# Performance work log

Hardware: AMD Instinct MI355X
Metric: run time of the kernel (lower is better)

Reference implementation:

```python
import jax, jax.numpy as jnp
from jax import lax
import numpy as np

H = 64  # hidden_dim


def _lstm_dir(x, W_ih, W_hh, b, reverse):
    # x: [B,T,I]; W_ih: [4H,I]; W_hh: [4H,H]; b: [4H] (b_ih+b_hh combined)
    B = x.shape[0]
    xp = jnp.einsum('bti,gi->btg', x, W_ih) + b          # [B,T,4H]
    xp = jnp.swapaxes(xp, 0, 1)                          # [T,B,4H]

    def step(carry, xt):
        h, c = carry
        g = xt + h @ W_hh.T                              # [B,4H]
        i, f, gg, o = jnp.split(g, 4, axis=-1)           # PyTorch gate order i,f,g,o
        i = jax.nn.sigmoid(i)
        f = jax.nn.sigmoid(f)
        gg = jnp.tanh(gg)
        o = jax.nn.sigmoid(o)
        c = f * c + i * gg
        h = o * jnp.tanh(c)
        return (h, c), h

    init = (jnp.zeros((B, H), x.dtype), jnp.zeros((B, H), x.dtype))
    _, hs = lax.scan(step, init, xp, reverse=reverse)    # outputs aligned to original positions
    return jnp.swapaxes(hs, 0, 1)                        # [B,T,H]


def _bilstm_layer(x, Wih_f, Whh_f, b_f, Wih_b, Whh_b, b_b):
    fwd = _lstm_dir(x, Wih_f, Whh_f, b_f, reverse=False)
    bwd = _lstm_dir(x, Wih_b, Whh_b, b_b, reverse=True)
    return jnp.concatenate([fwd, bwd], axis=-1)          # [B,T,2H]


def setup_inputs() -> dict:
    key = jax.random.key(0)
    ks = jax.random.split(key, 16)
    s = 0.1
    d = {}
    d['x'] = jax.random.normal(ks[0], (512, 512, 4), dtype=jnp.float32)
    # layer 0 (input size 4), forward / backward directions
    d['Wih_l0_f'] = jax.random.normal(ks[1], (4 * H, 4)) * s
    d['Whh_l0_f'] = jax.random.normal(ks[2], (4 * H, H)) * s
    d['b_l0_f'] = jax.random.normal(ks[3], (4 * H,)) * s
    d['Wih_l0_b'] = jax.random.normal(ks[4], (4 * H, 4)) * s
    d['Whh_l0_b'] = jax.random.normal(ks[5], (4 * H, H)) * s
    d['b_l0_b'] = jax.random.normal(ks[6], (4 * H,)) * s
    # layer 1 (input size 2H = 128)
    d['Wih_l1_f'] = jax.random.normal(ks[7], (4 * H, 2 * H)) * s
    d['Whh_l1_f'] = jax.random.normal(ks[8], (4 * H, H)) * s
    d['b_l1_f'] = jax.random.normal(ks[9], (4 * H,)) * s
    d['Wih_l1_b'] = jax.random.normal(ks[10], (4 * H, 2 * H)) * s
    d['Whh_l1_b'] = jax.random.normal(ks[11], (4 * H, H)) * s
    d['b_l1_b'] = jax.random.normal(ks[12], (4 * H,)) * s
    # final linear: 2H -> 1
    d['fc_w'] = jax.random.normal(ks[13], (1, 2 * H)) * s
    d['fc_b'] = jax.random.normal(ks[14], (1,)) * s
    return d


def reference(x, Wih_l0_f, Whh_l0_f, b_l0_f, Wih_l0_b, Whh_l0_b, b_l0_b,
              Wih_l1_f, Whh_l1_f, b_l1_f, Wih_l1_b, Whh_l1_b, b_l1_b,
              fc_w, fc_b):
    h0 = _bilstm_layer(x, Wih_l0_f, Whh_l0_f, b_l0_f, Wih_l0_b, Whh_l0_b, b_l0_b)
    h1 = _bilstm_layer(h0, Wih_l1_f, Whh_l1_f, b_l1_f, Wih_l1_b, Whh_l1_b, b_l1_b)
    pooled = jnp.mean(h1, axis=1)                        # [B,2H]
    return pooled @ fc_w.T + fc_b                        # [B,1]
```

## Files before the change

### kernel.cpp

```cpp
#include <hip/hip_runtime.h>

#define H  64
#define TT 512
#define BB 512
#define CSTR 80
#define UCH 16
#define XROW 264
#define XCH  (UCH * XROW + 8)
#define NCHUNK (TT / UCH)

typedef _Float16 half8 __attribute__((ext_vector_type(8)));
typedef float    f32x4 __attribute__((ext_vector_type(4)));

#define LOG2E 1.4426950408889634f
#define TWOL  2.8853900817779268f
#define FOURL 5.7707801635558536f

#define MFMA16 __builtin_amdgcn_mfma_f32_16x16x32_f16

__device__ __forceinline__ float frcp(float x) { return __builtin_amdgcn_rcpf(x); }
__device__ __forceinline__ float ex2(float x)  { return __builtin_amdgcn_exp2f(x); }

__device__ __forceinline__ void step_barrier() {
    asm volatile("s_waitcnt lgkmcnt(0)\n\ts_barrier" ::: "memory");
}

__device__ __forceinline__ float sel4(f32x4 v, bool lo, bool hi) {
    float a = lo ? v[1] : v[0];
    float b = lo ? v[3] : v[2];
    return hi ? b : a;
}

__global__ __launch_bounds__(256) void xpad_prep(const float* __restrict__ x,
                                                 _Float16* __restrict__ xpad) {
    int gid = blockIdx.x * 256 + threadIdx.x;
    int row = gid >> 2, q = gid & 3;
    half8 v = {0,0,0,0,0,0,0,0};
    if (q == 0) {
        float4 xv = ((const float4*)x)[row];
        v[0] = (_Float16)xv.x; v[1] = (_Float16)xv.y;
        v[2] = (_Float16)xv.z; v[3] = (_Float16)xv.w;
    }
    *(half8*)(xpad + (size_t)row * 32 + q * 8) = v;
}


#define L0_CHUNK(CIDX, XPR, XPW, AUSE, ALOAD)                                   \
    {                                                                           \
        const int c_ = (CIDX);                                                  \
        if (c_ + 2 < NCHUNK) {                                                  \
            const int tL = dir ? (TT - 1 - ((c_ + 2) * UCH + m))                \
                               : ((c_ + 2) * UCH + m);                          \
            _Pragma("unroll")                                                   \
            for (int cc = 0; cc < 4; ++cc)                                      \
                ALOAD[cc] = *(const half8*)(xpad +                              \
                    (size_t)((b0 + cc) * TT + tL) * 32 + q * 8);                \
        }                                                                       \
        _Pragma("unroll")                                                       \
        for (int u = 0; u < UCH; ++u) {                                         \
            half8 ah0 = *(const half8*)&hbuf[p][ch][q * 8];                     \
            half8 ah1 = *(const half8*)&hbuf[p][ch][32 + q * 8];                \
            f32x4 xq = *(const f32x4*)&XPR[ch * XCH + u * XROW + uo * 4];       \
            f32x4 g0 = MFMA16(Ah[0][0], ah0, vz, 0, 0, 0);                      \
            g0       = MFMA16(Ah[0][1], ah1, g0, 0, 0, 0);                      \
            f32x4 g1 = MFMA16(Ah[1][0], ah0, vz, 0, 0, 0);                      \
            g1       = MFMA16(Ah[1][1], ah1, g1, 0, 0, 0);                      \
            f32x4 g2 = MFMA16(Ah[2][0], ah0, vz, 0, 0, 0);                      \
            g2       = MFMA16(Ah[2][1], ah1, g2, 0, 0, 0);                      \
            f32x4 g3 = MFMA16(Ah[3][0], ah0, vz, 0, 0, 0);                      \
            g3       = MFMA16(Ah[3][1], ah1, g3, 0, 0, 0);                      \
            {                                \
                f32x4 acc = bb[u & 3];                                          \
                acc = MFMA16(Wg[u & 3], AUSE[u >> 2], acc, 0, 0, 0);            \
                *(f32x4*)&XPW[(u >> 2) * XCH + m * XROW +                       \
                              (w * 16 + (u & 3) * 4 + q) * 4] = acc;            \
            }                                                                   \
            float gi = sel4(g0, sLo, sHi) + xq[0];                              \
            float gf = sel4(g1, sLo, sHi) + xq[1];                              \
            float gg = sel4(g2, sLo, sHi) + xq[2];                              \
            float go = sel4(g3, sLo, sHi) + xq[3];                              \
            float e_i = frcp(1.f + ex2(gi));                                    \
            float e_f = frcp(1.f + ex2(gf));                                    \
            float tg  = TWOL - FOURL * frcp(1.f + ex2(gg));                     \
            float e_o = frcp(1.f + ex2(go));                                    \
            cp = e_f * cp + e_i * tg;                                           \
            float hh = e_o * fmaf(-2.f, frcp(1.f + ex2(cp)), 1.f);              \
            const int tg_t = dir ? (TT - 1 - (c_ * UCH + u)) : (c_ * UCH + u);  \
            out0[((size_t)(b0 + ch) * TT + tg_t) * 128 + dir * 64 + uo] =       \
                (_Float16)hh;                                                   \
            hbuf[p ^ 1][ch][uo] = (_Float16)hh;                                 \
            step_barrier();                                                     \
            p ^= 1;                                                             \
        }                                                                       \
    }

__global__ __launch_bounds__(256, 1) void lstm_l0(
    const _Float16* __restrict__ xpad,
    const float* __restrict__ WihF, const float* __restrict__ WhhF, const float* __restrict__ bF,
    const float* __restrict__ WihB, const float* __restrict__ WhhB, const float* __restrict__ bB,
    _Float16* __restrict__ out0)
{
    const int dir = blockIdx.x & 1;
    const int b0  = (blockIdx.x >> 1) * 4;
    const int tid = threadIdx.x;
    const int w = tid >> 6, l = tid & 63, m = l & 15, q = l >> 4;
    const int ch = m & 3;
    const int i0 = m >> 2;
    const int uo = w * 16 + q * 4 + i0;
    const bool sLo = (i0 & 1) != 0, sHi = (i0 & 2) != 0;

    const float* Wih = dir ? WihB : WihF;
    const float* Whh = dir ? WhhB : WhhF;
    const float* bia = dir ? bB   : bF;

    half8 Ah[4][2];
#pragma unroll
    for (int t = 0; t < 4; ++t) {
        const float st = (t == 2) ? TWOL : -LOG2E;
        const int wrow = t * 64 + w * 16 + m;
#pragma unroll
        for (int s2 = 0; s2 < 2; ++s2) {
            const float* src = Whh + wrow * 64 + s2 * 32 + q * 8;
            half8 tmp;
#pragma unroll
            for (int j = 0; j < 8; ++j) tmp[j] = (_Float16)(src[j] * st);
            Ah[t][s2] = tmp;
        }
    }

    const float sm = ((m & 3) == 2) ? TWOL : -LOG2E;
    half8 Wg[4];
#pragma unroll
    for (int j = 0; j < 4; ++j) {
        const int gr = (m & 3) * 64 + w * 16 + j * 4 + (m >> 2);
        half8 tmp;
#pragma unroll
        for (int jj = 0; jj < 8; ++jj) {
            int k = q * 8 + jj;
            tmp[jj] = (k < 4) ? (_Float16)(Wih[gr * 4 + k] * sm) : (_Float16)0.f;
        }
        Wg[j] = tmp;
    }

    f32x4 bb[4];
#pragma unroll
    for (int j = 0; j < 4; ++j) {
        const int ub = w * 16 + j * 4 + q;
        bb[j][0] = bia[ub]       * -LOG2E;
        bb[j][1] = bia[64 + ub]  * -LOG2E;
        bb[j][2] = bia[128 + ub] * TWOL;
        bb[j][3] = bia[192 + ub] * -LOG2E;
    }

    const f32x4 vz = {0.f, 0.f, 0.f, 0.f};

    __shared__ __align__(16) float xpA[4 * XCH];
    __shared__ __align__(16) float xpB[4 * XCH];
    __shared__ __align__(16) _Float16 hbuf[2][4][CSTR];
    for (int i = tid; i < 2 * 4 * CSTR / 2; i += 256) ((unsigned int*)hbuf)[i] = 0u;

    float cp = 0.f;
    int p = 0;

    half8 aR[2][4];
    {
        const int t0 = dir ? (TT - 1 - m) : m;
        const int t1 = dir ? (TT - 1 - (UCH + m)) : (UCH + m);
#pragma unroll
        for (int cc = 0; cc < 4; ++cc) {
            aR[0][cc] = *(const half8*)(xpad + (size_t)((b0 + cc) * TT + t0) * 32 + q * 8);
            aR[1][cc] = *(const half8*)(xpad + (size_t)((b0 + cc) * TT + t1) * 32 + q * 8);
        }
#pragma unroll
        for (int pp = 0; pp < 16; ++pp) {
            const int cc = pp >> 2, j = pp & 3;
            f32x4 acc = bb[j];
            acc = MFMA16(Wg[j], aR[0][cc], acc, 0, 0, 0);
            *(f32x4*)&xpA[cc * XCH + m * XROW + (w * 16 + j * 4 + q) * 4] = acc;
        }
        __syncthreads();
    }

    for (int c = 0; c < NCHUNK; c += 2) {
        L0_CHUNK(c,     xpA, xpB, aR[1], aR[0]);
        L0_CHUNK(c + 1, xpB, xpA, aR[0], aR[1]);
    }
}

#define L1_CHUNK(CIDX, XPR, XPW, AUSE, ALOAD)                                   \
    {                                                                           \
        const int c_ = (CIDX);                                                  \
        if (c_ + 2 < NCHUNK) {                                                  \
            const int tL = dir ? (TT - 1 - ((c_ + 2) * UCH + m))                \
                               : ((c_ + 2) * UCH + m);                          \
            _Pragma("unroll")                                                   \
            for (int cc = 0; cc < 4; ++cc) {                                    \
                const _Float16* arow = out0 +                                   \
                    (size_t)((b0 + cc) * TT + tL) * 128 + q * 8;                \
                _Pragma("unroll")                                               \
                for (int k4 = 0; k4 < 4; ++k4)                                  \
                    ALOAD[cc][k4] = *(const half8*)(arow + k4 * 32);            \
            }                                                                   \
        }                                                                       \
        _Pragma("unroll")                                                       \
        for (int u = 0; u < UCH; ++u) {                                         \
            half8 ah0 = *(const half8*)&hbuf[p][ch][q * 8];                     \
            half8 ah1 = *(const half8*)&hbuf[p][ch][32 + q * 8];                \
            f32x4 xq = *(const f32x4*)&XPR[ch * XCH + u * XROW + uo * 4];       \
            f32x4 g0 = MFMA16(Ah[0][0], ah0, vz, 0, 0, 0);                      \
            g0       = MFMA16(Ah[0][1], ah1, g0, 0, 0, 0);                      \
            f32x4 g1 = MFMA16(Ah[1][0], ah0, vz, 0, 0, 0);                      \
            g1       = MFMA16(Ah[1][1], ah1, g1, 0, 0, 0);                      \
            f32x4 g2 = MFMA16(Ah[2][0], ah0, vz, 0, 0, 0);                      \
            g2       = MFMA16(Ah[2][1], ah1, g2, 0, 0, 0);                      \
            f32x4 g3 = MFMA16(Ah[3][0], ah0, vz, 0, 0, 0);                      \
            g3       = MFMA16(Ah[3][1], ah1, g3, 0, 0, 0);                      \
            {                                   \
                f32x4 acc = bb[u & 3];                                          \
                acc = MFMA16(Wg[u & 3][0], AUSE[u >> 2][0], acc, 0, 0, 0);      \
                acc = MFMA16(Wg[u & 3][1], AUSE[u >> 2][1], acc, 0, 0, 0);      \
                acc = MFMA16(Wg[u & 3][2], AUSE[u >> 2][2], acc, 0, 0, 0);      \
                acc = MFMA16(Wg[u & 3][3], AUSE[u >> 2][3], acc, 0, 0, 0);      \
                *(f32x4*)&XPW[(u >> 2) * XCH + m * XROW +                       \
                              (w * 16 + (u & 3) * 4 + q) * 4] = acc;            \
            }                                                                   \
            float gi = sel4(g0, sLo, sHi) + xq[0];                              \
            float gf = sel4(g1, sLo, sHi) + xq[1];                              \
            float gg = sel4(g2, sLo, sHi) + xq[2];                              \
            float go = sel4(g3, sLo, sHi) + xq[3];                              \
            float e_i = frcp(1.f + ex2(gi));                                    \
            float e_f = frcp(1.f + ex2(gf));                                    \
            float tg  = TWOL - FOURL * frcp(1.f + ex2(gg));                     \
            float e_o = frcp(1.f + ex2(go));                                    \
            cp = e_f * cp + e_i * tg;                                           \
            float hh = e_o * fmaf(-2.f, frcp(1.f + ex2(cp)), 1.f);              \
            hs += hh;                                                           \
            hbuf[p ^ 1][ch][uo] = (_Float16)hh;                                 \
            step_barrier();                                                     \
            p ^= 1;                                                             \
        }                                                                       \
    }

__global__ __launch_bounds__(256, 1) void lstm_l1(
    const _Float16* __restrict__ out0,
    const float* __restrict__ WihF, const float* __restrict__ WhhF, const float* __restrict__ bF,
    const float* __restrict__ WihB, const float* __restrict__ WhhB, const float* __restrict__ bB,
    float* __restrict__ pooled)
{
    const int dir = blockIdx.x & 1;
    const int b0  = (blockIdx.x >> 1) * 4;
    const int tid = threadIdx.x;
    const int w = tid >> 6, l = tid & 63, m = l & 15, q = l >> 4;
    const int ch = m & 3;
    const int i0 = m >> 2;
    const int uo = w * 16 + q * 4 + i0;
    const bool sLo = (i0 & 1) != 0, sHi = (i0 & 2) != 0;

    const float* Wih = dir ? WihB : WihF;
    const float* Whh = dir ? WhhB : WhhF;
    const float* bia = dir ? bB   : bF;

    half8 Ah[4][2];
#pragma unroll
    for (int t = 0; t < 4; ++t) {
        const float st = (t == 2) ? TWOL : -LOG2E;
        const int wrow = t * 64 + w * 16 + m;
#pragma unroll
        for (int s2 = 0; s2 < 2; ++s2) {
            const float* src = Whh + wrow * 64 + s2 * 32 + q * 8;
            half8 tmp;
#pragma unroll
            for (int j = 0; j < 8; ++j) tmp[j] = (_Float16)(src[j] * st);
            Ah[t][s2] = tmp;
        }
    }

    const float sm = ((m & 3) == 2) ? TWOL : -LOG2E;
    half8 Wg[4][4];
#pragma unroll
    for (int j = 0; j < 4; ++j) {
        const int gr = (m & 3) * 64 + w * 16 + j * 4 + (m >> 2);
#pragma unroll
        for (int k4 = 0; k4 < 4; ++k4) {
            const float* src = Wih + gr * 128 + k4 * 32 + q * 8;
            half8 tmp;
#pragma unroll
            for (int jj = 0; jj < 8; ++jj) tmp[jj] = (_Float16)(src[jj] * sm);
            Wg[j][k4] = tmp;
        }
    }

    f32x4 bb[4];
#pragma unroll
    for (int j = 0; j < 4; ++j) {
        const int ub = w * 16 + j * 4 + q;
        bb[j][0] = bia[ub]       * -LOG2E;
        bb[j][1] = bia[64 + ub]  * -LOG2E;
        bb[j][2] = bia[128 + ub] * TWOL;
        bb[j][3] = bia[192 + ub] * -LOG2E;
    }

    const f32x4 vz = {0.f, 0.f, 0.f, 0.f};

    __shared__ __align__(16) float xpA[4 * XCH];
    __shared__ __align__(16) float xpB[4 * XCH];
    __shared__ __align__(16) _Float16 hbuf[2][4][CSTR];
    for (int i = tid; i < 2 * 4 * CSTR / 2; i += 256) ((unsigned int*)hbuf)[i] = 0u;

    float cp = 0.f, hs = 0.f;
    int p = 0;

    half8 aR[2][4][4];
    {
        const int t0 = dir ? (TT - 1 - m) : m;
        const int t1 = dir ? (TT - 1 - (UCH + m)) : (UCH + m);
#pragma unroll
        for (int cc = 0; cc < 4; ++cc) {
            const _Float16* r0 = out0 + (size_t)((b0 + cc) * TT + t0) * 128 + q * 8;
            const _Float16* r1 = out0 + (size_t)((b0 + cc) * TT + t1) * 128 + q * 8;
#pragma unroll
            for (int k4 = 0; k4 < 4; ++k4) {
                aR[0][cc][k4] = *(const half8*)(r0 + k4 * 32);
                aR[1][cc][k4] = *(const half8*)(r1 + k4 * 32);
            }
        }
#pragma unroll
        for (int pp = 0; pp < 16; ++pp) {
            const int cc = pp >> 2, j = pp & 3;
            f32x4 acc = bb[j];
            acc = MFMA16(Wg[j][0], aR[0][cc][0], acc, 0, 0, 0);
            acc = MFMA16(Wg[j][1], aR[0][cc][1], acc, 0, 0, 0);
            acc = MFMA16(Wg[j][2], aR[0][cc][2], acc, 0, 0, 0);
            acc = MFMA16(Wg[j][3], aR[0][cc][3], acc, 0, 0, 0);
            *(f32x4*)&xpA[cc * XCH + m * XROW + (w * 16 + j * 4 + q) * 4] = acc;
        }
        __syncthreads();
    }

    for (int c = 0; c < NCHUNK; c += 2) {
        L1_CHUNK(c,     xpA, xpB, aR[1], aR[0]);
        L1_CHUNK(c + 1, xpB, xpA, aR[0], aR[1]);
    }

    pooled[(size_t)(b0 + ch) * 128 + dir * 64 + uo] = hs;
}

__global__ __launch_bounds__(64) void fc_head(
    const float* __restrict__ pooled,
    const float* __restrict__ fcw, const float* __restrict__ fcb,
    float* __restrict__ out)
{
    const int b = blockIdx.x;
    const int l = threadIdx.x;
    float v = pooled[b * 128 + l] * fcw[l] + pooled[b * 128 + 64 + l] * fcw[64 + l];
#pragma unroll
    for (int o = 32; o > 0; o >>= 1) v += __shfl_down(v, o);
    if (l == 0) out[b] = v * (1.f / (float)TT) + fcb[0];
}

extern "C" void kernel_launch(void* const* d_in, const int* in_sizes, int n_in,
                              void* d_out, int out_size, void* d_ws, size_t ws_size,
                              hipStream_t stream) {
    const float* x       = (const float*)d_in[0];
    const float* Wih_l0f = (const float*)d_in[1];
    const float* Whh_l0f = (const float*)d_in[2];
    const float* b_l0f   = (const float*)d_in[3];
    const float* Wih_l0b = (const float*)d_in[4];
    const float* Whh_l0b = (const float*)d_in[5];
    const float* b_l0b   = (const float*)d_in[6];
    const float* Wih_l1f = (const float*)d_in[7];
    const float* Whh_l1f = (const float*)d_in[8];
    const float* b_l1f   = (const float*)d_in[9];
    const float* Wih_l1b = (const float*)d_in[10];
    const float* Whh_l1b = (const float*)d_in[11];
    const float* b_l1b   = (const float*)d_in[12];
    const float* fcw     = (const float*)d_in[13];
    const float* fcb     = (const float*)d_in[14];

    const size_t o_xpad   = 0;
    const size_t o_out0   = o_xpad + (size_t)BB * TT * 32 * 2;
    const size_t o_pooled = o_out0 + (size_t)BB * TT * 128 * 2;

    _Float16* xpad   = (_Float16*)((char*)d_ws + o_xpad);
    _Float16* out0   = (_Float16*)((char*)d_ws + o_out0);
    float*    pooled = (float*)((char*)d_ws + o_pooled);

    xpad_prep<<<(BB * TT * 4) / 256, 256, 0, stream>>>(x, xpad);
    lstm_l0<<<(BB / 4) * 2, 256, 0, stream>>>(xpad, Wih_l0f, Whh_l0f, b_l0f,
                                              Wih_l0b, Whh_l0b, b_l0b, out0);
    lstm_l1<<<(BB / 4) * 2, 256, 0, stream>>>(out0, Wih_l1f, Whh_l1f, b_l1f,
                                              Wih_l1b, Whh_l1b, b_l1b, pooled);
    fc_head<<<BB, 64, 0, stream>>>(pooled, fcw, fcb, (float*)d_out);
}
```

Measured before the change: 401.8 us.

## Swizzle LDS gate-projection layout and fuse LSTM activation reciprocals

Replaces the padded per-chunk LDS layout for the precomputed input projections with a per-wave block layout that uses XOR swizzling, aiming to cut LDS bank conflicts on both the writes and the per-step reads. Rewrites the gate nonlinearity so each pair of sigmoid/tanh reciprocals becomes one combined reciprocal, removing transcendental operations from the serial recurrence. In layer 1 the four-deep MFMA accumulation chain is split into two independent chains to shorten dependency latency. The fused activation may overflow for large exponent products, which could change numerics.

After: 414.9 us. 1.03x slower.

```diff
diff --git a/kernel.cpp b/kernel.cpp
--- a/kernel.cpp
+++ b/kernel.cpp
@@ -5,16 +5,17 @@
 #define BB 512
 #define CSTR 80
 #define UCH 16
-#define XROW 264
-#define XCH  (UCH * XROW + 8)
 #define NCHUNK (TT / UCH)
+
+#define WBLK 4096
+#define SBLK 256
+#define CBLK 64
 
 typedef _Float16 half8 __attribute__((ext_vector_type(8)));
 typedef float    f32x4 __attribute__((ext_vector_type(4)));
 
 #define LOG2E 1.4426950408889634f
 #define TWOL  2.8853900817779268f
-#define FOURL 5.7707801635558536f
 
 #define MFMA16 __builtin_amdgcn_mfma_f32_16x16x32_f16
 
@@ -44,6 +45,17 @@
     *(half8*)(xpad + (size_t)row * 32 + q * 8) = v;
 }
 
+
+#define FUSED_ACT()                                                             \
+    float I = ex2(gi), F = ex2(gf), G = ex2(gg), O = ex2(go);                   \
+    float i1 = 1.f + I;                                                         \
+    float rIG = frcp(fmaf(i1, G, i1));                                          \
+    float P   = fmaf(TWOL, G, -TWOL) * rIG;           \
+    cp = fmaf(frcp(1.f + F), cp, P);                                            \
+    float Cx = ex2(cp);                                                         \
+    float o1 = 1.f + O;                                                         \
+    float rOC = frcp(fmaf(o1, Cx, o1));                                         \
+    float hh = (Cx - 1.f) * rOC;
 
 #define L0_CHUNK(CIDX, XPR, XPW, AUSE, ALOAD)                                   \
     {                                                                           \
@@ -60,7 +72,8 @@
         for (int u = 0; u < UCH; ++u) {                                         \
             half8 ah0 = *(const half8*)&hbuf[p][ch][q * 8];                     \
             half8 ah1 = *(const half8*)&hbuf[p][ch][32 + q * 8];                \
-            f32x4 xq = *(const f32x4*)&XPR[ch * XCH + u * XROW + uo * 4];       \
+            f32x4 xq = *(const f32x4*)&XPR[rbase + u * SBLK +                   \
+                                           ((ul ^ (u & 7)) << 2)];              \
             f32x4 g0 = MFMA16(Ah[0][0], ah0, vz, 0, 0, 0);                      \
             g0       = MFMA16(Ah[0][1], ah1, g0, 0, 0, 0);                      \
             f32x4 g1 = MFMA16(Ah[1][0], ah0, vz, 0, 0, 0);                      \
@@ -69,22 +82,16 @@
             g2       = MFMA16(Ah[2][1], ah1, g2, 0, 0, 0);                      \
             f32x4 g3 = MFMA16(Ah[3][0], ah0, vz, 0, 0, 0);                      \
             g3       = MFMA16(Ah[3][1], ah1, g3, 0, 0, 0);                      \
-            {                                \
-                f32x4 acc = bb[u & 3];                                          \
-                acc = MFMA16(Wg[u & 3], AUSE[u >> 2], acc, 0, 0, 0);            \
-                *(f32x4*)&XPW[(u >> 2) * XCH + m * XROW +                       \
-                              (w * 16 + (u & 3) * 4 + q) * 4] = acc;            \
+            {       \
+                f32x4 acc = MFMA16(Wg[u & 3], AUSE[u >> 2], bb[u & 3], 0,0,0);  \
+                *(f32x4*)&XPW[wq + (u >> 2) * CBLK +                            \
+                              ((((u & 3) * 4 + q) ^ mk) << 2)] = acc;           \
             }                                                                   \
             float gi = sel4(g0, sLo, sHi) + xq[0];                              \
             float gf = sel4(g1, sLo, sHi) + xq[1];                              \
             float gg = sel4(g2, sLo, sHi) + xq[2];                              \
             float go = sel4(g3, sLo, sHi) + xq[3];                              \
-            float e_i = frcp(1.f + ex2(gi));                                    \
-            float e_f = frcp(1.f + ex2(gf));                                    \
-            float tg  = TWOL - FOURL * frcp(1.f + ex2(gg));                     \
-            float e_o = frcp(1.f + ex2(go));                                    \
-            cp = e_f * cp + e_i * tg;                                           \
-            float hh = e_o * fmaf(-2.f, frcp(1.f + ex2(cp)), 1.f);              \
+            FUSED_ACT()                                                         \
             const int tg_t = dir ? (TT - 1 - (c_ * UCH + u)) : (c_ * UCH + u);  \
             out0[((size_t)(b0 + ch) * TT + tg_t) * 128 + dir * 64 + uo] =       \
                 (_Float16)hh;                                                   \
@@ -106,7 +113,11 @@
     const int w = tid >> 6, l = tid & 63, m = l & 15, q = l >> 4;
     const int ch = m & 3;
     const int i0 = m >> 2;
-    const int uo = w * 16 + q * 4 + i0;
+    const int ul = q * 4 + i0;
+    const int uo = w * 16 + ul;
+    const int mk = m & 7;
+    const int rbase = w * WBLK + ch * CBLK;
+    const int wq    = w * WBLK + m * SBLK;
     const bool sLo = (i0 & 1) != 0, sHi = (i0 & 2) != 0;
 
     const float* Wih = dir ? WihB : WihF;
@@ -154,8 +165,8 @@
 
     const f32x4 vz = {0.f, 0.f, 0.f, 0.f};
 
-    __shared__ __align__(16) float xpA[4 * XCH];
-    __shared__ __align__(16) float xpB[4 * XCH];
+    __shared__ __align__(16) float xpA[4 * WBLK];
+    __shared__ __align__(16) float xpB[4 * WBLK];
     __shared__ __align__(16) _Float16 hbuf[2][4][CSTR];
     for (int i = tid; i < 2 * 4 * CSTR / 2; i += 256) ((unsigned int*)hbuf)[i] = 0u;
 
@@ -174,9 +185,8 @@
 #pragma unroll
         for (int pp = 0; pp < 16; ++pp) {
             const int cc = pp >> 2, j = pp & 3;
-            f32x4 acc = bb[j];
-            acc = MFMA16(Wg[j], aR[0][cc], acc, 0, 0, 0);
-            *(f32x4*)&xpA[cc * XCH + m * XROW + (w * 16 + j * 4 + q) * 4] = acc;
+            f32x4 acc = MFMA16(Wg[j], aR[0][cc], bb[j], 0, 0, 0);
+            *(f32x4*)&xpA[wq + cc * CBLK + (((j * 4 + q) ^ mk) << 2)] = acc;
         }
         __syncthreads();
     }
@@ -206,7 +216,8 @@
         for (int u = 0; u < UCH; ++u) {                                         \
             half8 ah0 = *(const half8*)&hbuf[p][ch][q * 8];                     \
             half8 ah1 = *(const half8*)&hbuf[p][ch][32 + q * 8];                \
-            f32x4 xq = *(const f32x4*)&XPR[ch * XCH + u * XROW + uo * 4];       \
+            f32x4 xq = *(const f32x4*)&XPR[rbase + u * SBLK +                   \
+                                           ((ul ^ (u & 7)) << 2)];              \
             f32x4 g0 = MFMA16(Ah[0][0], ah0, vz, 0, 0, 0);                      \
             g0       = MFMA16(Ah[0][1], ah1, g0, 0, 0, 0);                      \
             f32x4 g1 = MFMA16(Ah[1][0], ah0, vz, 0, 0, 0);                      \
@@ -215,25 +226,20 @@
             g2       = MFMA16(Ah[2][1], ah1, g2, 0, 0, 0);                      \
             f32x4 g3 = MFMA16(Ah[3][0], ah0, vz, 0, 0, 0);                      \
             g3       = MFMA16(Ah[3][1], ah1, g3, 0, 0, 0);                      \
-            {                                   \
-                f32x4 acc = bb[u & 3];                                          \
-                acc = MFMA16(Wg[u & 3][0], AUSE[u >> 2][0], acc, 0, 0, 0);      \
-                acc = MFMA16(Wg[u & 3][1], AUSE[u >> 2][1], acc, 0, 0, 0);      \
-                acc = MFMA16(Wg[u & 3][2], AUSE[u >> 2][2], acc, 0, 0, 0);      \
-                acc = MFMA16(Wg[u & 3][3], AUSE[u >> 2][3], acc, 0, 0, 0);      \
-                *(f32x4*)&XPW[(u >> 2) * XCH + m * XROW +                       \
-                              (w * 16 + (u & 3) * 4 + q) * 4] = acc;            \
+            {       \
+                f32x4 pA = MFMA16(Wg[u & 3][0], AUSE[u >> 2][0], bb[u & 3], 0,0,0); \
+                pA       = MFMA16(Wg[u & 3][1], AUSE[u >> 2][1], pA, 0, 0, 0);  \
+                f32x4 pB = MFMA16(Wg[u & 3][2], AUSE[u >> 2][2], vz, 0, 0, 0);  \
+                pB       = MFMA16(Wg[u & 3][3], AUSE[u >> 2][3], pB, 0, 0, 0);  \
+                f32x4 acc = pA + pB;                                            \
+                *(f32x4*)&XPW[wq + (u >> 2) * CBLK +                            \
+                              ((((u & 3) * 4 + q) ^ mk) << 2)] = acc;           \
             }                                                                   \
             float gi = sel4(g0, sLo, sHi) + xq[0];                              \
             float gf = sel4(g1, sLo, sHi) + xq[1];                              \
             float gg = sel4(g2, sLo, sHi) + xq[2];                              \
             float go = sel4(g3, sLo, sHi) + xq[3];                              \
-            float e_i = frcp(1.f + ex2(gi));                                    \
-            float e_f = frcp(1.f + ex2(gf));                                    \
-            float tg  = TWOL - FOURL * frcp(1.f + ex2(gg));                     \
-            float e_o = frcp(1.f + ex2(go));                                    \
-            cp = e_f * cp + e_i * tg;                                           \
-            float hh = e_o * fmaf(-2.f, frcp(1.f + ex2(cp)), 1.f);              \
+            FUSED_ACT()                                                         \
             hs += hh;                                                           \
             hbuf[p ^ 1][ch][uo] = (_Float16)hh;                                 \
             step_barrier();                                                     \
@@ -253,7 +259,11 @@
     const int w = tid >> 6, l = tid & 63, m = l & 15, q = l >> 4;
     const int ch = m & 3;
     const int i0 = m >> 2;
-    const int uo = w * 16 + q * 4 + i0;
+    const int ul = q * 4 + i0;
+    const int uo = w * 16 + ul;
+    const int mk = m & 7;
+    const int rbase = w * WBLK + ch * CBLK;
+    const int wq    = w * WBLK + m * SBLK;
     const bool sLo = (i0 & 1) != 0, sHi = (i0 & 2) != 0;
 
     const float* Wih = dir ? WihB : WihF;
@@ -302,8 +312,8 @@
 
     const f32x4 vz = {0.f, 0.f, 0.f, 0.f};
 
-    __shared__ __align__(16) float xpA[4 * XCH];
-    __shared__ __align__(16) float xpB[4 * XCH];
+    __shared__ __align__(16) float xpA[4 * WBLK];
+    __shared__ __align__(16) float xpB[4 * WBLK];
     __shared__ __align__(16) _Float16 hbuf[2][4][CSTR];
     for (int i = tid; i < 2 * 4 * CSTR / 2; i += 256) ((unsigned int*)hbuf)[i] = 0u;
 
@@ -327,12 +337,11 @@
 #pragma unroll
         for (int pp = 0; pp < 16; ++pp) {
             const int cc = pp >> 2, j = pp & 3;
-            f32x4 acc = bb[j];
-            acc = MFMA16(Wg[j][0], aR[0][cc][0], acc, 0, 0, 0);
+            f32x4 acc = MFMA16(Wg[j][0], aR[0][cc][0], bb[j], 0, 0, 0);
             acc = MFMA16(Wg[j][1], aR[0][cc][1], acc, 0, 0, 0);
             acc = MFMA16(Wg[j][2], aR[0][cc][2], acc, 0, 0, 0);
             acc = MFMA16(Wg[j][3], aR[0][cc][3], acc, 0, 0, 0);
-            *(f32x4*)&xpA[cc * XCH + m * XROW + (w * 16 + j * 4 + q) * 4] = acc;
+            *(f32x4*)&xpA[wq + cc * CBLK + (((j * 4 + q) ^ mk) << 2)] = acc;
         }
         __syncthreads();
     }
```
